# Kernel tuning notes

Measured on AMD Instinct MI355X. Metric: run time of the kernel, lower is better.

## Reference

```python
import jax, jax.numpy as jnp
import numpy as np

B, S, H, I, E, K = 2, 512, 768, 3072, 8, 1
LB_COEF = 0.01


def _xavier(key, shape, fan_in, fan_out):
    limit = np.sqrt(6.0 / (fan_in + fan_out)).astype(np.float32)
    return jax.random.uniform(key, shape, jnp.float32, -limit, limit)


def setup_inputs() -> dict:
    key = jax.random.key(0)
    k0, k1, k2, k3 = jax.random.split(key, 4)
    return {
        "hidden_states": jax.random.normal(k0, (B, S, H), jnp.float32),
        "gate_w": _xavier(k1, (E, H), H, E),          # nn.Linear(H, E).weight
        "gate_b": jnp.zeros((E,), jnp.float32),
        "w1": _xavier(k2, (E, I, H), H, I),           # per-expert Linear(H, I).weight
        "b1": jnp.zeros((E, I), jnp.float32),
        "w2": _xavier(k3, (E, H, I), I, H),           # per-expert Linear(I, H).weight
        "b2": jnp.zeros((E, H), jnp.float32),
    }


def reference(hidden_states, gate_w, gate_b, w1, b1, w2, b2):
    b, s, h = hidden_states.shape
    x = hidden_states.reshape(-1, h)                      # [T, H]
    gate_logits = x @ gate_w.T + gate_b                   # [T, E]
    top_vals, top_idx = jax.lax.top_k(gate_logits, K)     # [T, K]
    # softmax over the (single) selected logit in fp32 -> all ones, kept for fidelity
    gate_weights = jax.nn.softmax(top_vals.astype(jnp.float32), axis=-1)  # [T, K]

    # load balancing loss (torch.var is unbiased, ddof=1)
    gate_mean = gate_logits.mean(axis=0)                  # [E]
    gate_var = gate_logits.var(axis=0, ddof=1)            # [E]
    lb_loss = LB_COEF * (gate_var / (gate_mean ** 2 + 1e-8)).mean()

    # dense per-expert FFN (exact math; combine picks the routed expert)
    hmid = jnp.einsum('th,eih->tei', x, w1) + b1          # [T, E, I]
    hmid = jax.nn.gelu(hmid, approximate=False)           # torch nn.GELU (erf)
    y = jnp.einsum('tei,ehi->teh', hmid, w2) + b2         # [T, E, H]

    sel = top_idx[:, 0]                                   # [T]
    y_sel = jnp.take_along_axis(y, sel[:, None, None], axis=1)[:, 0]  # [T, H]
    out = y_sel * gate_weights[:, 0:1]                    # weight == 1.0 for k=1
    return out.reshape(b, s, h), lb_loss
```

## Files before the change

kernel.cpp:

```cpp
#include <hip/hip_runtime.h>
#include <hip/hip_bf16.h>
#include <math.h>

#define Hdim 768
#define Idim 3072
#define Tn   1024
#define En   8
#define CAP  256
#define LD1  72
#define LD2  136

using v4f     = __attribute__((ext_vector_type(4))) float;
using short8  = __attribute__((ext_vector_type(8))) short;
using short4v = __attribute__((ext_vector_type(4))) short;

__device__ inline unsigned short f2bf(float f) {
    unsigned u = __float_as_uint(f);
    u += 0x7fffu + ((u >> 16) & 1u);
    return (unsigned short)(u >> 16);
}
__device__ inline short4v pack4(float4 v) {
    return short4v{ (short)f2bf(v.x), (short)f2bf(v.y), (short)f2bf(v.z), (short)f2bf(v.w) };
}
__device__ __forceinline__ void gl2lds16(const unsigned short* g, unsigned short* l) {
    __builtin_amdgcn_global_load_lds(
        (const __attribute__((address_space(1))) void*)g,
        (__attribute__((address_space(3))) void*)l, 16, 0, 0);
}

__global__ __launch_bounds__(256) void gate_kernel(
    const float* __restrict__ x, const float* __restrict__ gw, const float* __restrict__ gb,
    float* __restrict__ psum, float* __restrict__ psumsq,
    int* __restrict__ sel, int* __restrict__ gcur)
{
    __shared__ float gws[8 * 772];
    __shared__ float lg[8][8];
    int tid = threadIdx.x;
    long t0 = (long)blockIdx.x * 8;
    if (blockIdx.x == 0 && tid < En) gcur[tid] = 0;
    for (int i = tid; i < 8 * 768; i += 256) gws[(i / 768) * 772 + (i % 768)] = gw[i];
    __syncthreads();

    int tok = tid >> 5, e = (tid >> 2) & 7, qr = tid & 3;
    const float4* xp = (const float4*)(x + (t0 + tok) * Hdim) + qr * 48;
    const float4* gp = (const float4*)(gws + e * 772) + qr * 48;
    float a0 = 0.f, a1 = 0.f;
#pragma unroll 8
    for (int i = 0; i < 48; i += 2) {
        float4 xa = xp[i], ga = gp[i], xc = xp[i + 1], gc = gp[i + 1];
        a0 += xa.x * ga.x + xa.y * ga.y + xa.z * ga.z + xa.w * ga.w;
        a1 += xc.x * gc.x + xc.y * gc.y + xc.z * gc.z + xc.w * gc.w;
    }
    float acc = a0 + a1;
    acc += __shfl_xor(acc, 1);
    acc += __shfl_xor(acc, 2);
    if (qr == 0) lg[tok][e] = acc + gb[e];
    __syncthreads();

    if (tid < 8) {
        float best = lg[tid][0]; int bi = 0;
        for (int j = 1; j < 8; j++) { float v = lg[tid][j]; if (v > best) { best = v; bi = j; } }
        sel[t0 + tid] = bi;
    } else if (tid < 16) {
        int e2 = tid - 8;
        float s = 0.f, ss = 0.f;
        for (int t2 = 0; t2 < 8; t2++) { float v = lg[t2][e2]; s += v; ss += v * v; }
        psum[blockIdx.x * 8 + e2]   = s;
        psumsq[blockIdx.x * 8 + e2] = ss;
    }
}

__global__ __launch_bounds__(256) void gather_kernel(
    const float* __restrict__ x, const int* __restrict__ sel,
    const float* __restrict__ psum, const float* __restrict__ psumsq,
    int* __restrict__ gcur, int* __restrict__ perm,
    unsigned short* __restrict__ xb, float* __restrict__ out_lb)
{
    int tid = threadIdx.x;
    if (blockIdx.x == 0 && tid < 64) {
        int e = tid & 7, c0 = (tid >> 3) * 16;
        float s = 0.f, ss = 0.f;
        for (int b = c0; b < c0 + 16; b++) { s += psum[b * 8 + e]; ss += psumsq[b * 8 + e]; }
        s  += __shfl_xor(s, 8);  s  += __shfl_xor(s, 16);  s  += __shfl_xor(s, 32);
        ss += __shfl_xor(ss, 8); ss += __shfl_xor(ss, 16); ss += __shfl_xor(ss, 32);
        if (tid < 8) {
            float mean = s * (1.0f / 1024.0f);
            float var  = (ss - s * mean) * (1.0f / 1023.0f);
            float r = var / (mean * mean + 1e-8f);
            r += __shfl_xor(r, 1); r += __shfl_xor(r, 2); r += __shfl_xor(r, 4);
            if (tid == 0) out_lb[0] = 0.01f * r * 0.125f;
        }
    }
    int t = blockIdx.x * 4 + (tid >> 6);
    int lane = tid & 63;
    int e = sel[t];
    int pos = 0;
    if (lane == 0) pos = atomicAdd(&gcur[e], 1);
    pos = __shfl(pos, 0);
    if (pos < CAP) {
        int slot = (e << 8) + pos;
        if (lane == 0) perm[slot] = t;
        const float4* src = (const float4*)(x + (long)t * Hdim);
        unsigned short* dst = xb + (long)slot * Hdim;
#pragma unroll
        for (int i = 0; i < 3; i++) {
            int c = lane + 64 * i;
            *(short4v*)(dst + c * 4) = pack4(src[c]);
        }
    }
}

__global__ __launch_bounds__(256) void gemm1_kernel(
    const unsigned short* __restrict__ xb, const float* __restrict__ w1, const float* __restrict__ b1,
    const int* __restrict__ count, unsigned short* __restrict__ hmid)
{
    int e = blockIdx.z;
    int nloc = count[e]; if (nloc > CAP) nloc = CAP;
    int m0 = blockIdx.y << 6;
    if (m0 >= nloc) return;
    int n0 = blockIdx.x << 5;
    int off = e << 8;

    __shared__ __align__(16) unsigned short As[64 * 64];
    __shared__ __align__(16) unsigned short Bs[32 * LD1];

    int tid = threadIdx.x;
    int lane = tid & 63, wave = tid >> 6;
    int quad = lane >> 4, l16 = lane & 15;
    int wm = wave << 4;

    const unsigned short* aG[2];
    unsigned short* aL[2];
#pragma unroll
    for (int i = 0; i < 2; i++) {
        int p = (wave * 2 + i) * 64 + lane;
        int row = p >> 3;
        int kc = (p & 7) ^ (row & 7);
        int m = m0 + row; int mm = m < nloc ? m : nloc - 1;
        aG[i] = xb + (long)(off + mm) * Hdim + kc * 8;
        aL[i] = (unsigned short*)As + p * 8;
    }
    int kq = tid & 15, rb = tid >> 4;
    const float* bp0 = w1 + ((long)e * Idim + n0 + rb) * Hdim + kq * 4;
    const float* bp1 = bp0 + (long)16 * Hdim;

    v4f acc[2];
    acc[0] = (v4f){0.f, 0.f, 0.f, 0.f};
    acc[1] = (v4f){0.f, 0.f, 0.f, 0.f};

    float4 nb0 = *(const float4*)bp0;
    float4 nb1 = *(const float4*)bp1;

    for (int kb = 0; kb < Hdim; kb += 64) {
        __syncthreads();
#pragma unroll
        for (int i = 0; i < 2; i++) gl2lds16(aG[i] + kb, aL[i]);
        *(short4v*)(Bs + rb * LD1 + kq * 4)        = pack4(nb0);
        *(short4v*)(Bs + (rb + 16) * LD1 + kq * 4) = pack4(nb1);
        __syncthreads();
        if (kb + 64 < Hdim) {
            nb0 = *(const float4*)(bp0 + kb + 64);
            nb1 = *(const float4*)(bp1 + kb + 64);
        }
#pragma unroll
        for (int s = 0; s < 2; s++) {
            int r = wm + l16;
            short8 af = *(const short8*)(As + r * 64 + (((s * 4 + quad) ^ (r & 7)) * 8));
            short8 bf2[2];
#pragma unroll
            for (int j = 0; j < 2; j++)
                bf2[j] = *(const short8*)(Bs + (j * 16 + l16) * LD1 + s * 32 + quad * 8);
#pragma unroll
            for (int j = 0; j < 2; j++)
                acc[j] = __builtin_amdgcn_mfma_f32_16x16x32_bf16(af, bf2[j], acc[j], 0, 0, 0);
        }
    }

    int mr = wm + quad * 4;
#pragma unroll
    for (int r = 0; r < 4; r++) {
        int m = m0 + mr + r;
        if (m >= nloc) continue;
        long slot = off + m;
#pragma unroll
        for (int j = 0; j < 2; j++) {
            int n = n0 + j * 16 + l16;
            float v = acc[j][r] + b1[e * Idim + n];
            float g = 0.5f * v * (1.0f + erff(v * 0.70710678118654752f));
            hmid[slot * Idim + n] = f2bf(g);
        }
    }
}

__global__ __launch_bounds__(256) void gemm2_kernel(
    const unsigned short* __restrict__ hmid, const float* __restrict__ w2,
    const float* __restrict__ b2,
    const int* __restrict__ count, const int* __restrict__ perm,
    float* __restrict__ out)
{
    int e = blockIdx.z;
    int nloc = count[e]; if (nloc > CAP) nloc = CAP;
    int m0 = blockIdx.y << 6;
    if (m0 >= nloc) return;
    int n0 = blockIdx.x << 5;
    int off = e << 8;

    __shared__ __align__(16) unsigned short As[64 * 128];
    __shared__ __align__(16) unsigned short Bs[32 * LD2];

    int tid = threadIdx.x;
    int lane = tid & 63, wave = tid >> 6;
    int quad = lane >> 4, l16 = lane & 15;
    int wm = wave << 4;

    const unsigned short* aG[4];
    unsigned short* aL[4];
#pragma unroll
    for (int i = 0; i < 4; i++) {
        int p = (wave * 4 + i) * 64 + lane;
        int row = p >> 4;
        int kc = (p & 15) ^ (row & 15);
        int m = m0 + row; int mm = m < nloc ? m : nloc - 1;
        aG[i] = hmid + (long)(off + mm) * Idim + kc * 8;
        aL[i] = (unsigned short*)As + p * 8;
    }
    int kq5 = tid & 31, rb8 = tid >> 5;
    const float* bp[4];
#pragma unroll
    for (int s = 0; s < 4; s++)
        bp[s] = w2 + ((long)e * Hdim + n0 + rb8 + 8 * s) * Idim + kq5 * 4;

    v4f acc[2];
    acc[0] = (v4f){0.f, 0.f, 0.f, 0.f};
    acc[1] = (v4f){0.f, 0.f, 0.f, 0.f};

    float4 nb[4];
#pragma unroll
    for (int s = 0; s < 4; s++) nb[s] = *(const float4*)bp[s];

    for (int kb = 0; kb < Idim; kb += 128) {
        __syncthreads();
#pragma unroll
        for (int i = 0; i < 4; i++) gl2lds16(aG[i] + kb, aL[i]);
#pragma unroll
        for (int s = 0; s < 4; s++)
            *(short4v*)(Bs + (rb8 + 8 * s) * LD2 + kq5 * 4) = pack4(nb[s]);
        __syncthreads();
        if (kb + 128 < Idim) {
#pragma unroll
            for (int s = 0; s < 4; s++) nb[s] = *(const float4*)(bp[s] + kb + 128);
        }
#pragma unroll
        for (int s = 0; s < 4; s++) {
            int r = wm + l16;
            short8 af = *(const short8*)(As + r * 128 + (((s * 4 + quad) ^ (r & 15)) * 8));
            short8 bf2[2];
#pragma unroll
            for (int j = 0; j < 2; j++)
                bf2[j] = *(const short8*)(Bs + (j * 16 + l16) * LD2 + s * 32 + quad * 8);
#pragma unroll
            for (int j = 0; j < 2; j++)
                acc[j] = __builtin_amdgcn_mfma_f32_16x16x32_bf16(af, bf2[j], acc[j], 0, 0, 0);
        }
    }

    int mr = wm + quad * 4;
#pragma unroll
    for (int r = 0; r < 4; r++) {
        int m = m0 + mr + r;
        if (m >= nloc) continue;
        int t = perm[off + m];
#pragma unroll
        for (int j = 0; j < 2; j++) {
            int n = n0 + j * 16 + l16;
            out[(long)t * Hdim + n] = acc[j][r] + b2[e * Hdim + n];
        }
    }
}

extern "C" void kernel_launch(void* const* d_in, const int* in_sizes, int n_in,
                              void* d_out, int out_size, void* d_ws, size_t ws_size,
                              hipStream_t stream)
{
    const float* x  = (const float*)d_in[0];
    const float* gw = (const float*)d_in[1];
    const float* gb = (const float*)d_in[2];
    const float* w1 = (const float*)d_in[3];
    const float* b1 = (const float*)d_in[4];
    const float* w2 = (const float*)d_in[5];
    const float* b2 = (const float*)d_in[6];
    float* out = (float*)d_out;

    int*   gcur   = (int*)d_ws;
    int*   sel    = (int*)((char*)d_ws + 128);
    float* psum   = (float*)((char*)d_ws + 4352);
    float* psumsq = (float*)((char*)d_ws + 8448);
    int*   perm   = (int*)((char*)d_ws + 12544);
    unsigned short* xb   = (unsigned short*)((char*)d_ws + 32768);
    unsigned short* hmid = (unsigned short*)((char*)d_ws + (1u << 22));

    gate_kernel  <<<128, 256, 0, stream>>>(x, gw, gb, psum, psumsq, sel, gcur);
    gather_kernel<<<256, 256, 0, stream>>>(x, sel, psum, psumsq, gcur, perm, xb,
                                           out + (long)Tn * Hdim);
    gemm1_kernel <<<dim3(96, 4, 8), 256, 0, stream>>>(xb, w1, b1, gcur, hmid);
    gemm2_kernel <<<dim3(24, 4, 8), 256, 0, stream>>>(hmid, w2, b2, gcur, perm, out);
}
```

Before: 234.4 us.

## Split-K gemm2 into four partial slabs with a bias-adding reduce kernel

The second expert GEMM now splits its 3072-long K dimension into four chunks of 768. This quadruples the grid from 768 to 3072 blocks so more of the GPU is busy. Each chunk writes fp32 partials to a workspace, and a new reduce kernel sums the four partials, adds the routed expert bias and writes the output. Separately, gemm1 moves to 128-wide K tiles with the same swizzled LDS layout as gemm2, which halves its barrier count. The cost is about 12 MB of extra partial-sum traffic and one more kernel launch.

```diff
diff --git a/kernel.cpp b/kernel.cpp
--- a/kernel.cpp
+++ b/kernel.cpp
@@ -7,7 +7,6 @@
 #define Tn   1024
 #define En   8
 #define CAP  256
-#define LD1  72
 #define LD2  136
 
 using v4f     = __attribute__((ext_vector_type(4))) float;
@@ -121,55 +120,59 @@
     int n0 = blockIdx.x << 5;
     int off = e << 8;
 
-    __shared__ __align__(16) unsigned short As[64 * 64];
-    __shared__ __align__(16) unsigned short Bs[32 * LD1];
+    __shared__ __align__(16) unsigned short As[64 * 128];
+    __shared__ __align__(16) unsigned short Bs[32 * LD2];
 
     int tid = threadIdx.x;
     int lane = tid & 63, wave = tid >> 6;
     int quad = lane >> 4, l16 = lane & 15;
     int wm = wave << 4;
 
-    const unsigned short* aG[2];
-    unsigned short* aL[2];
-#pragma unroll
-    for (int i = 0; i < 2; i++) {
-        int p = (wave * 2 + i) * 64 + lane;
-        int row = p >> 3;
-        int kc = (p & 7) ^ (row & 7);
+    const unsigned short* aG[4];
+    unsigned short* aL[4];
+#pragma unroll
+    for (int i = 0; i < 4; i++) {
+        int p = (wave * 4 + i) * 64 + lane;
+        int row = p >> 4;
+        int kc = (p & 15) ^ (row & 15);
         int m = m0 + row; int mm = m < nloc ? m : nloc - 1;
         aG[i] = xb + (long)(off + mm) * Hdim + kc * 8;
         aL[i] = (unsigned short*)As + p * 8;
     }
-    int kq = tid & 15, rb = tid >> 4;
-    const float* bp0 = w1 + ((long)e * Idim + n0 + rb) * Hdim + kq * 4;
-    const float* bp1 = bp0 + (long)16 * Hdim;
+    int kq5 = tid & 31, rb8 = tid >> 5;
+    const float* bp[4];
+#pragma unroll
+    for (int s = 0; s < 4; s++)
+        bp[s] = w1 + ((long)e * Idim + n0 + rb8 + 8 * s) * Hdim + kq5 * 4;
 
     v4f acc[2];
     acc[0] = (v4f){0.f, 0.f, 0.f, 0.f};
     acc[1] = (v4f){0.f, 0.f, 0.f, 0.f};
 
-    float4 nb0 = *(const float4*)bp0;
-    float4 nb1 = *(const float4*)bp1;
-
-    for (int kb = 0; kb < Hdim; kb += 64) {
+    float4 nb[4];
+#pragma unroll
+    for (int s = 0; s < 4; s++) nb[s] = *(const float4*)bp[s];
+
+    for (int kb = 0; kb < Hdim; kb += 128) {
         __syncthreads();
 #pragma unroll
-        for (int i = 0; i < 2; i++) gl2lds16(aG[i] + kb, aL[i]);
-        *(short4v*)(Bs + rb * LD1 + kq * 4)        = pack4(nb0);
-        *(short4v*)(Bs + (rb + 16) * LD1 + kq * 4) = pack4(nb1);
+        for (int i = 0; i < 4; i++) gl2lds16(aG[i] + kb, aL[i]);
+#pragma unroll
+        for (int s = 0; s < 4; s++)
+            *(short4v*)(Bs + (rb8 + 8 * s) * LD2 + kq5 * 4) = pack4(nb[s]);
         __syncthreads();
-        if (kb + 64 < Hdim) {
-            nb0 = *(const float4*)(bp0 + kb + 64);
-            nb1 = *(const float4*)(bp1 + kb + 64);
-        }
-#pragma unroll
-        for (int s = 0; s < 2; s++) {
+        if (kb + 128 < Hdim) {
+#pragma unroll
+            for (int s = 0; s < 4; s++) nb[s] = *(const float4*)(bp[s] + kb + 128);
+        }
+#pragma unroll
+        for (int s = 0; s < 4; s++) {
             int r = wm + l16;
-            short8 af = *(const short8*)(As + r * 64 + (((s * 4 + quad) ^ (r & 7)) * 8));
+            short8 af = *(const short8*)(As + r * 128 + (((s * 4 + quad) ^ (r & 15)) * 8));
             short8 bf2[2];
 #pragma unroll
             for (int j = 0; j < 2; j++)
-                bf2[j] = *(const short8*)(Bs + (j * 16 + l16) * LD1 + s * 32 + quad * 8);
+                bf2[j] = *(const short8*)(Bs + (j * 16 + l16) * LD2 + s * 32 + quad * 8);
 #pragma unroll
             for (int j = 0; j < 2; j++)
                 acc[j] = __builtin_amdgcn_mfma_f32_16x16x32_bf16(af, bf2[j], acc[j], 0, 0, 0);
@@ -194,15 +197,17 @@
 
 __global__ __launch_bounds__(256) void gemm2_kernel(
     const unsigned short* __restrict__ hmid, const float* __restrict__ w2,
-    const float* __restrict__ b2,
     const int* __restrict__ count, const int* __restrict__ perm,
-    float* __restrict__ out)
+    float* __restrict__ parts)
 {
     int e = blockIdx.z;
     int nloc = count[e]; if (nloc > CAP) nloc = CAP;
     int m0 = blockIdx.y << 6;
     if (m0 >= nloc) return;
-    int n0 = blockIdx.x << 5;
+    int bx = blockIdx.x;
+    int n0 = (bx % 24) << 5;
+    int kc4 = bx / 24;
+    long kbase = (long)kc4 * 768;
     int off = e << 8;
 
     __shared__ __align__(16) unsigned short As[64 * 128];
@@ -221,14 +226,14 @@
         int row = p >> 4;
         int kc = (p & 15) ^ (row & 15);
         int m = m0 + row; int mm = m < nloc ? m : nloc - 1;
-        aG[i] = hmid + (long)(off + mm) * Idim + kc * 8;
+        aG[i] = hmid + (long)(off + mm) * Idim + kbase + kc * 8;
         aL[i] = (unsigned short*)As + p * 8;
     }
     int kq5 = tid & 31, rb8 = tid >> 5;
     const float* bp[4];
 #pragma unroll
     for (int s = 0; s < 4; s++)
-        bp[s] = w2 + ((long)e * Hdim + n0 + rb8 + 8 * s) * Idim + kq5 * 4;
+        bp[s] = w2 + ((long)e * Hdim + n0 + rb8 + 8 * s) * Idim + kbase + kq5 * 4;
 
     v4f acc[2];
     acc[0] = (v4f){0.f, 0.f, 0.f, 0.f};
@@ -238,7 +243,7 @@
 #pragma unroll
     for (int s = 0; s < 4; s++) nb[s] = *(const float4*)bp[s];
 
-    for (int kb = 0; kb < Idim; kb += 128) {
+    for (int kb = 0; kb < 768; kb += 128) {
         __syncthreads();
 #pragma unroll
         for (int i = 0; i < 4; i++) gl2lds16(aG[i] + kb, aL[i]);
@@ -246,7 +251,7 @@
         for (int s = 0; s < 4; s++)
             *(short4v*)(Bs + (rb8 + 8 * s) * LD2 + kq5 * 4) = pack4(nb[s]);
         __syncthreads();
-        if (kb + 128 < Idim) {
+        if (kb + 128 < 768) {
 #pragma unroll
             for (int s = 0; s < 4; s++) nb[s] = *(const float4*)(bp[s] + kb + 128);
         }
@@ -264,6 +269,7 @@
         }
     }
 
+    float* pout = parts + (long)kc4 * Tn * Hdim;
     int mr = wm + quad * 4;
 #pragma unroll
     for (int r = 0; r < 4; r++) {
@@ -273,9 +279,30 @@
 #pragma unroll
         for (int j = 0; j < 2; j++) {
             int n = n0 + j * 16 + l16;
-            out[(long)t * Hdim + n] = acc[j][r] + b2[e * Hdim + n];
-        }
-    }
+            pout[(long)t * Hdim + n] = acc[j][r];
+        }
+    }
+}
+
+__global__ __launch_bounds__(256) void reduce_kernel(
+    const float* __restrict__ parts, const float* __restrict__ b2,
+    const int* __restrict__ sel, float* __restrict__ out)
+{
+    int idx = blockIdx.x * 256 + threadIdx.x;
+    int t = idx / 192, n4 = idx - t * 192;
+    int e = sel[t];
+    const float4* p = (const float4*)parts;
+    float4 a = p[idx];
+    float4 b = p[idx + 196608];
+    float4 c = p[idx + 2 * 196608];
+    float4 d = p[idx + 3 * 196608];
+    float4 bias = ((const float4*)(b2 + (long)e * Hdim))[n4];
+    float4 r;
+    r.x = a.x + b.x + c.x + d.x + bias.x;
+    r.y = a.y + b.y + c.y + d.y + bias.y;
+    r.z = a.z + b.z + c.z + d.z + bias.z;
+    r.w = a.w + b.w + c.w + d.w + bias.w;
+    ((float4*)out)[idx] = r;
 }
 
 extern "C" void kernel_launch(void* const* d_in, const int* in_sizes, int n_in,
@@ -298,10 +325,12 @@
     int*   perm   = (int*)((char*)d_ws + 12544);
     unsigned short* xb   = (unsigned short*)((char*)d_ws + 32768);
     unsigned short* hmid = (unsigned short*)((char*)d_ws + (1u << 22));
+    float* parts = (float*)((char*)d_ws + (1u << 25));
 
     gate_kernel  <<<128, 256, 0, stream>>>(x, gw, gb, psum, psumsq, sel, gcur);
     gather_kernel<<<256, 256, 0, stream>>>(x, sel, psum, psumsq, gcur, perm, xb,
                                            out + (long)Tn * Hdim);
     gemm1_kernel <<<dim3(96, 4, 8), 256, 0, stream>>>(xb, w1, b1, gcur, hmid);
-    gemm2_kernel <<<dim3(24, 4, 8), 256, 0, stream>>>(hmid, w2, b2, gcur, perm, out);
-}
+    gemm2_kernel <<<dim3(96, 4, 8), 256, 0, stream>>>(hmid, w2, gcur, perm, parts);
+    reduce_kernel<<<768, 256, 0, stream>>>(parts, b2, sel, out);
+}
```

New measurement: 236.5 us. About the same (+0.9%).
